# Optimization experiments

Hardware: AMD Instinct MI355X
Metric: run time of the kernel (lower is better)

Reference implementation:

```python
import jax, jax.numpy as jnp
import numpy as np

N, E, B, ROWS, IN, HID, JKO, FEAT, OH, OUT = 200000, 6400000, 64, 128, 128, 6, 4, 2560, 20, 2

def _leaky(x, s):
    return jnp.where(x >= 0, x, s * x)

def _ln(x, g, b, eps=1e-5):
    mu = jnp.mean(x, -1, keepdims=True)
    v = jnp.mean((x - mu) ** 2, -1, keepdims=True)
    return (x - mu) * jax.lax.rsqrt(v + eps) * g + b

def setup_inputs():
    key = jax.random.key(0)
    ks = jax.random.split(key, 32)
    def w(k, shape, fan_in):
        return jax.random.normal(k, shape, jnp.float32) * (1.0 / np.sqrt(fan_in))
    inp = {
        'x': jax.random.normal(ks[0], (N, IN), jnp.float32),
        'edge_index': jax.random.randint(ks[1], (2, E), 0, N, jnp.int32),
        'batch': jnp.sort(jax.random.randint(ks[2], (N,), 0, B, jnp.int32)),
        'features': jax.random.normal(ks[3], (B, ROWS, FEAT), jnp.float32),
        'one_hot': jax.random.uniform(ks[4], (B, OH), jnp.float32),
        # GATv2Conv params (heads=1)
        'W_l': w(ks[5], (IN, HID), IN), 'b_l': jnp.zeros((HID,)),
        'W_r': w(ks[6], (IN, HID), IN), 'b_r': jnp.zeros((HID,)),
        'att': w(ks[7], (HID,), HID), 'conv_b': jnp.zeros((HID,)),
        # BasicGNN final lin after JK (6 -> 4)
        'jk_W': w(ks[8], (HID, JKO), HID), 'jk_b': jnp.zeros((JKO,)),
        # MLP chain on features
        'l1_W': w(ks[9], (FEAT, 256), FEAT), 'l1_b': jnp.zeros((256,)),
        'ln1_g': jnp.ones((256,)), 'ln1_b': jnp.zeros((256,)),
        'l2_W': w(ks[10], (256, 64), 256), 'l2_b': jnp.zeros((64,)),
        'ln2_g': jnp.ones((64,)), 'ln2_b': jnp.zeros((64,)),
        'l3_W': w(ks[11], (64, 8), 64), 'l3_b': jnp.zeros((8,)),
        'ln3_g': jnp.ones((8,)), 'ln3_b': jnp.zeros((8,)),
        # flattening: rows*8 -> 32
        'fl_W': w(ks[12], (ROWS * 8, 32), ROWS * 8), 'fl_b': jnp.zeros((32,)),
        'ln4_g': jnp.ones((32,)), 'ln4_b': jnp.zeros((32,)),
        # output: 4 + 32 + 20 = 56 -> OUT
        'out_W': w(ks[13], (56, OUT), 56), 'out_b': jnp.zeros((OUT,)),
    }
    return inp

def _forward(x, features, one_hot, W_l, b_l, W_r, b_r, att, conv_b, jk_W, jk_b,
             l1_W, l1_b, ln1_g, ln1_b, l2_W, l2_b, ln2_g, ln2_b, l3_W, l3_b, ln3_g, ln3_b,
             fl_W, fl_b, ln4_g, ln4_b, out_W, out_b, edge_index, batch):
    n = x.shape[0]
    # GATv2Conv, heads=1: separate source/target transforms
    xl = x @ W_l + b_l  # [N,6] source/message features
    xr = x @ W_r + b_r  # [N,6] target features
    loops = jnp.arange(n, dtype=edge_index.dtype)
    src = jnp.concatenate([edge_index[0], loops])  # add self loops
    dst = jnp.concatenate([edge_index[1], loops])
    e = _leaky(xl[src] + xr[dst], 0.2)             # [E+N,6]
    score = e @ att                                 # [E+N]
    m = jax.lax.stop_gradient(jax.ops.segment_max(score, dst, num_segments=n))
    p = jnp.exp(score - m[dst])
    z = jax.ops.segment_sum(p, dst, num_segments=n)
    alpha = p / z[dst]                              # segment softmax over incoming edges
    agg = jax.ops.segment_sum(alpha[:, None] * xl[src], dst, num_segments=n) + conv_b
    x1 = _leaky(agg, 0.01)                          # BasicGNN act ('leakyrelu')
    # JK-LSTM with a single layer collapses to identity (softmax over 1 element)
    h = x1 @ jk_W + jk_b                            # [N,4]
    # global mean pool per graph
    nb = features.shape[0]
    sums = jax.ops.segment_sum(h, batch, num_segments=nb)
    cnt = jax.ops.segment_sum(jnp.ones((n,), h.dtype), batch, num_segments=nb)
    xgcn = sums / jnp.maximum(cnt, 1.0)[:, None]    # [B,4]
    # MLP on features (dropout = identity in eval)
    f = _leaky(_ln(features @ l1_W + l1_b, ln1_g, ln1_b), 0.01)
    f = _leaky(_ln(f @ l2_W + l2_b, ln2_g, ln2_b), 0.01)
    f = _leaky(_ln(f @ l3_W + l3_b, ln3_g, ln3_b), 0.01)  # [B,ROWS,8]
    flat = f.reshape(nb, -1)
    xf = _leaky(_ln(flat @ fl_W + fl_b, ln4_g, ln4_b), 0.01)  # [B,32]
    cat = jnp.concatenate([xgcn, xf, one_hot], axis=1)        # [B,56]
    return cat @ out_W + out_b

def reference(x, features, one_hot, W_l, b_l, W_r, b_r, att, conv_b, jk_W, jk_b,
              l1_W, l1_b, ln1_g, ln1_b, l2_W, l2_b, ln2_g, ln2_b, l3_W, l3_b, ln3_g, ln3_b,
              fl_W, fl_b, ln4_g, ln4_b, out_W, out_b, edge_index, batch):
    return _forward(x, features, one_hot, W_l, b_l, W_r, b_r, att, conv_b, jk_W, jk_b,
                    l1_W, l1_b, ln1_g, ln1_b, l2_W, l2_b, ln2_g, ln2_b, l3_W, l3_b, ln3_g, ln3_b,
                    fl_W, fl_b, ln4_g, ln4_b, out_W, out_b, edge_index, batch)
```

## Files before the change

### kernel.cpp

```cpp
#include <hip/hip_runtime.h>
#include <cstdint>
#include <cstddef>

#define N_NODES 200000
#define N_EDGES 6400000
#define NB      64
#define MROWS   8192
#define FEAT    2560

#define BSZ   256
#define NBK   782
#define EBLK  512
#define ETILE 12500
#define BCAP  8960

typedef __attribute__((ext_vector_type(8))) short bf16x8;
typedef __attribute__((ext_vector_type(4))) float f32x4;

__device__ __forceinline__ unsigned short bf16rne(float f) {
    unsigned u = __builtin_bit_cast(unsigned, f);
    u += 0x7fffu + ((u >> 16) & 1u);
    return (unsigned short)(u >> 16);
}

__device__ __forceinline__ void async_cp16(const void* g, void* l) {
    __builtin_amdgcn_global_load_lds(
        (const __attribute__((address_space(1))) unsigned int*)g,
        (__attribute__((address_space(3))) unsigned int*)l, 16, 0, 0);
}

__device__ __forceinline__ void edge_acc(
    uint4 g, const float* xrd, const float* attv, float& z, float* agg)
{
    float xls[6];
    xls[0] = __builtin_bit_cast(float, g.x << 16);
    xls[1] = __builtin_bit_cast(float, g.x & 0xffff0000u);
    xls[2] = __builtin_bit_cast(float, g.y << 16);
    xls[3] = __builtin_bit_cast(float, g.y & 0xffff0000u);
    xls[4] = __builtin_bit_cast(float, g.z << 16);
    xls[5] = __builtin_bit_cast(float, g.z & 0xffff0000u);
    float sc = 0.f;
#pragma unroll
    for (int j = 0; j < 6; j++) {
        float e = xls[j] + xrd[j];
        e = (e >= 0.f) ? e : 0.2f * e;
        sc += attv[j] * e;
    }
    const float p = __expf(sc);
    z += p;
#pragma unroll
    for (int j = 0; j < 6; j++) agg[j] += p * xls[j];
}


__global__ __launch_bounds__(256) void node_xform(
    const float* __restrict__ x,
    const float* __restrict__ Wl, const float* __restrict__ bl,
    const float* __restrict__ Wr, const float* __restrict__ br,
    unsigned short* __restrict__ xlb, float* __restrict__ xr)
{
    const int t = threadIdx.x;
    const int l = t & 15;
    const int node = blockIdx.x * 16 + (t >> 4);

    float wl[48], wr[48];
#pragma unroll
    for (int q = 0; q < 12; q++) {
        *(float4*)&wl[q * 4] = *(const float4*)(Wl + 48 * l + 4 * q);
        *(float4*)&wr[q * 4] = *(const float4*)(Wr + 48 * l + 4 * q);
    }
    float xv[8];
    *(float4*)&xv[0] = *(const float4*)(x + (size_t)node * 128 + l * 8);
    *(float4*)&xv[4] = *(const float4*)(x + (size_t)node * 128 + l * 8 + 4);

    float al[6] = {}, ar[6] = {};
#pragma unroll
    for (int i = 0; i < 8; i++) {
#pragma unroll
        for (int j = 0; j < 6; j++) {
            al[j] += xv[i] * wl[i * 6 + j];
            ar[j] += xv[i] * wr[i * 6 + j];
        }
    }
#pragma unroll
    for (int off = 8; off >= 1; off >>= 1) {
#pragma unroll
        for (int j = 0; j < 6; j++) {
            al[j] += __shfl_xor(al[j], off);
            ar[j] += __shfl_xor(ar[j], off);
        }
    }
    if (l == 0) {
        union { unsigned short h[8]; uint4 v; } u;
#pragma unroll
        for (int j = 0; j < 6; j++) u.h[j] = bf16rne(al[j] + bl[j]);
        u.h[6] = 0; u.h[7] = 0;
        *(uint4*)(xlb + (size_t)node * 8) = u.v;
        float4 r0; float2 r1;
        r0.x = ar[0] + br[0]; r0.y = ar[1] + br[1];
        r0.z = ar[2] + br[2]; r0.w = ar[3] + br[3];
        r1.x = ar[4] + br[4]; r1.y = ar[5] + br[5];
        *(float4*)(xr + (size_t)node * 8) = r0;
        *(float2*)(xr + (size_t)node * 8 + 4) = r1;
    }
}

__global__ __launch_bounds__(256) void edge_bucket(
    const int* __restrict__ ei, int* __restrict__ cursor, int* __restrict__ pairs)
{
    __shared__ int dcache[ETILE];
    __shared__ int h[NBK];
    const int t = threadIdx.x;
    const int base = blockIdx.x * ETILE;
    for (int i = t; i < NBK; i += 256) h[i] = 0;
    __syncthreads();
    for (int i = t; i < ETILE; i += 256) {
        const int d = ei[N_EDGES + base + i];
        dcache[i] = d;
        atomicAdd(&h[d >> 8], 1);
    }
    __syncthreads();
    for (int b = t; b < NBK; b += 256) {
        const int c = h[b];
        int gb = 0;
        if (c > 0) gb = atomicAdd(&cursor[b], c);
        h[b] = b * BCAP + gb;
    }
    __syncthreads();
    for (int i = t; i < ETILE; i += 256) {
        const int d = dcache[i];
        const int s = ei[base + i];
        const int pos = atomicAdd(&h[d >> 8], 1);
        pairs[pos] = (s << 8) | (d & 255);
    }
}

__global__ __launch_bounds__(256) void bucket_reduce(
    const int* __restrict__ pairs, const int* __restrict__ cursor,
    const unsigned short* __restrict__ xlb, const float* __restrict__ xr,
    const float* __restrict__ att, const float* __restrict__ conv_b,
    const float* __restrict__ jkW, const float* __restrict__ jkb,
    const int* __restrict__ batch,
    float* __restrict__ gsum, float* __restrict__ gcnt)
{
    __shared__ int sorted[BCAP];
    __shared__ int hist[256];
    __shared__ int wtot[4];
    const int t = threadIdx.x;
    const int lane = t & 63, wid = t >> 6;
    const int d0 = blockIdx.x * BSZ + t;

    float xrd[6];
    if (d0 < N_NODES) {
        float4 a = *(const float4*)(xr + (size_t)d0 * 8);
        float2 b = *(const float2*)(xr + (size_t)d0 * 8 + 4);
        xrd[0] = a.x; xrd[1] = a.y; xrd[2] = a.z;
        xrd[3] = a.w; xrd[4] = b.x; xrd[5] = b.y;
    } else {
#pragma unroll
        for (int j = 0; j < 6; j++) xrd[j] = 0.f;
    }
    float attv[6];
#pragma unroll
    for (int j = 0; j < 6; j++) attv[j] = att[j];

    float z = 0.f, agg[6] = {};
    const uint4* xl4 = (const uint4*)xlb;
    const int e0 = blockIdx.x * BCAP;
    const int e1 = e0 + cursor[blockIdx.x];

    for (int c0 = e0; c0 < e1; c0 += BCAP) {
        const int rem = e1 - c0;
        const int cnt_chunk = (rem < BCAP) ? rem : BCAP;
        hist[t] = 0;
        __syncthreads();
        for (int i = t; i < cnt_chunk; i += 256)
            atomicAdd(&hist[pairs[c0 + i] & 255], 1);
        __syncthreads();
        const int h = hist[t];
        int v = h;
#pragma unroll
        for (int d = 1; d < 64; d <<= 1) {
            int o = __shfl_up(v, d);
            if (lane >= d) v += o;
        }
        if (lane == 63) wtot[wid] = v;
        __syncthreads();
        int off = 0;
#pragma unroll
        for (int wv = 0; wv < 3; wv++) if (wv < wid) off += wtot[wv];
        const int my_start = v - h + off;
        const int my_cnt = h;
        __syncthreads();
        hist[t] = my_start;
        __syncthreads();
        for (int i = t; i < cnt_chunk; i += 256) {
            const int pv = pairs[c0 + i];
            const int pos = atomicAdd(&hist[pv & 255], 1);
            sorted[pos] = ((unsigned)pv) >> 8;
        }
        __syncthreads();
        int i = 0;
        for (; i + 4 <= my_cnt; i += 4) {
            const int s0 = sorted[my_start + i];
            const int s1 = sorted[my_start + i + 1];
            const int s2 = sorted[my_start + i + 2];
            const int s3 = sorted[my_start + i + 3];
            const uint4 g0 = xl4[s0], g1 = xl4[s1], g2 = xl4[s2], g3 = xl4[s3];
            edge_acc(g0, xrd, attv, z, agg);
            edge_acc(g1, xrd, attv, z, agg);
            edge_acc(g2, xrd, attv, z, agg);
            edge_acc(g3, xrd, attv, z, agg);
        }
        for (; i < my_cnt; i++) {
            const uint4 g = xl4[sorted[my_start + i]];
            edge_acc(g, xrd, attv, z, agg);
        }
        __syncthreads();
    }

    float hh[4] = {0.f, 0.f, 0.f, 0.f};
    float cw = 0.f;
    int b = 0;
    if (d0 < N_NODES) {
        const uint4 g = xl4[d0];
        float xld[6];
        xld[0] = __builtin_bit_cast(float, g.x << 16);
        xld[1] = __builtin_bit_cast(float, g.x & 0xffff0000u);
        xld[2] = __builtin_bit_cast(float, g.y << 16);
        xld[3] = __builtin_bit_cast(float, g.y & 0xffff0000u);
        xld[4] = __builtin_bit_cast(float, g.z << 16);
        xld[5] = __builtin_bit_cast(float, g.z & 0xffff0000u);
        float sc = 0.f;
#pragma unroll
        for (int j = 0; j < 6; j++) {
            float e = xld[j] + xrd[j];
            e = (e >= 0.f) ? e : 0.2f * e;
            sc += attv[j] * e;
        }
        const float p = __expf(sc);
        const float zz = z + p;
#pragma unroll
        for (int c = 0; c < 4; c++) hh[c] = jkb[c];
#pragma unroll
        for (int j = 0; j < 6; j++) {
            float aj = (agg[j] + p * xld[j]) / zz + conv_b[j];
            aj = (aj >= 0.f) ? aj : 0.01f * aj;
#pragma unroll
            for (int c = 0; c < 4; c++) hh[c] += aj * jkW[j * 4 + c];
        }
        b = batch[d0];
        cw = 1.f;
    }
    const int b0 = __shfl(b, 0);
    if (__all(b == b0)) {
#pragma unroll
        for (int off2 = 32; off2 >= 1; off2 >>= 1) {
#pragma unroll
            for (int c = 0; c < 4; c++) hh[c] += __shfl_xor(hh[c], off2);
            cw += __shfl_xor(cw, off2);
        }
        if (lane == 0 && cw > 0.f) {
#pragma unroll
            for (int c = 0; c < 4; c++) atomicAdd(gsum + b0 * 4 + c, hh[c]);
            atomicAdd(gcnt + b0, cw);
        }
    } else if (cw > 0.f) {
#pragma unroll
        for (int c = 0; c < 4; c++) atomicAdd(gsum + b * 4 + c, hh[c]);
        atomicAdd(gcnt + b, cw);
    }
}

__global__ __launch_bounds__(256) void castT(
    const float* __restrict__ W, unsigned short* __restrict__ Wt, int K, int N)
{
    const int k = blockIdx.x * 256 + threadIdx.x;
    const int n = blockIdx.y;
    if (k < K) Wt[(size_t)n * K + k] = bf16rne(W[(size_t)k * N + n]);
}

__global__ __launch_bounds__(256) void mfma_gemm_l1(
    const float* __restrict__ A, const unsigned short* __restrict__ Bt,
    const float* __restrict__ bias, float* __restrict__ C,
    int M, int N, int K)
{
    __shared__ unsigned short As[2][64 * 64];
    __shared__ unsigned short Bs[2][128 * 64];
    const int t = threadIdx.x;
    const int w = t >> 6, l = t & 63;
    const int l15 = l & 15, quad = l >> 4;
    const int wm = (w & 1) * 32, wn = (w >> 1) * 64;
    const int gm0 = blockIdx.x * 64;
    const int gn0 = blockIdx.y * 128;
    const int r8 = l >> 3;
    const int c8 = (l & 7) ^ r8;
    const int ar = t >> 2;
    const int ac0 = (t & 3) * 2;

    f32x4 acc[2][4];
#pragma unroll
    for (int mt = 0; mt < 2; mt++)
#pragma unroll
        for (int nt = 0; nt < 4; nt++) acc[mt][nt] = (f32x4){0.f, 0.f, 0.f, 0.f};

    const int niter = K / 64;

#pragma unroll
    for (int c = 0; c < 4; c++) {
        const int j = w * 4 + c;
        async_cp16(Bt + (size_t)(gn0 + j * 8 + r8) * K + c8 * 8, &Bs[0][j * 512]);
    }
    {
        const float* src = A + (size_t)(gm0 + ar) * K + ac0 * 8;
        float4 v0 = *(const float4*)src;
        float4 v1 = *(const float4*)(src + 4);
        float4 v2 = *(const float4*)(src + 8);
        float4 v3 = *(const float4*)(src + 12);
        union { unsigned short h[8]; uint4 u; } p0, p1;
        p0.h[0] = bf16rne(v0.x); p0.h[1] = bf16rne(v0.y);
        p0.h[2] = bf16rne(v0.z); p0.h[3] = bf16rne(v0.w);
        p0.h[4] = bf16rne(v1.x); p0.h[5] = bf16rne(v1.y);
        p0.h[6] = bf16rne(v1.z); p0.h[7] = bf16rne(v1.w);
        p1.h[0] = bf16rne(v2.x); p1.h[1] = bf16rne(v2.y);
        p1.h[2] = bf16rne(v2.z); p1.h[3] = bf16rne(v2.w);
        p1.h[4] = bf16rne(v3.x); p1.h[5] = bf16rne(v3.y);
        p1.h[6] = bf16rne(v3.z); p1.h[7] = bf16rne(v3.w);
        *(uint4*)&As[0][ar * 64 + ((ac0 + 0) ^ (ar & 7)) * 8] = p0.u;
        *(uint4*)&As[0][ar * 64 + ((ac0 + 1) ^ (ar & 7)) * 8] = p1.u;
    }

    int p = 0;
    for (int i = 0; i < niter; i++) {
        __syncthreads();
        const bool nxt = (i + 1 < niter);
        float4 v0, v1, v2, v3;
        if (nxt) {
            const int k1 = (i + 1) * 64;
#pragma unroll
            for (int c = 0; c < 4; c++) {
                const int j = w * 4 + c;
                async_cp16(Bt + (size_t)(gn0 + j * 8 + r8) * K + k1 + c8 * 8,
                           &Bs[p ^ 1][j * 512]);
            }
            const float* src = A + (size_t)(gm0 + ar) * K + k1 + ac0 * 8;
            v0 = *(const float4*)src;
            v1 = *(const float4*)(src + 4);
            v2 = *(const float4*)(src + 8);
            v3 = *(const float4*)(src + 12);
        }
#pragma unroll
        for (int kki = 0; kki < 2; kki++) {
            bf16x8 af[2], bfr[4];
#pragma unroll
            for (int mt = 0; mt < 2; mt++) {
                const int m = wm + mt * 16 + l15;
                af[mt] = *(const bf16x8*)&As[p][m * 64 + (((quad + 4 * kki) ^ (m & 7)) * 8)];
            }
#pragma unroll
            for (int nt = 0; nt < 4; nt++) {
                const int n = wn + nt * 16 + l15;
                bfr[nt] = *(const bf16x8*)&Bs[p][n * 64 + (((quad + 4 * kki) ^ (n & 7)) * 8)];
            }
#pragma unroll
            for (int mt = 0; mt < 2; mt++)
#pragma unroll
                for (int nt = 0; nt < 4; nt++)
                    acc[mt][nt] = __builtin_amdgcn_mfma_f32_16x16x32_bf16(
                        af[mt], bfr[nt], acc[mt][nt], 0, 0, 0);
        }
        if (nxt) {
            union { unsigned short h[8]; uint4 u; } p0, p1;
            p0.h[0] = bf16rne(v0.x); p0.h[1] = bf16rne(v0.y);
            p0.h[2] = bf16rne(v0.z); p0.h[3] = bf16rne(v0.w);
            p0.h[4] = bf16rne(v1.x); p0.h[5] = bf16rne(v1.y);
            p0.h[6] = bf16rne(v1.z); p0.h[7] = bf16rne(v1.w);
            p1.h[0] = bf16rne(v2.x); p1.h[1] = bf16rne(v2.y);
            p1.h[2] = bf16rne(v2.z); p1.h[3] = bf16rne(v2.w);
            p1.h[4] = bf16rne(v3.x); p1.h[5] = bf16rne(v3.y);
            p1.h[6] = bf16rne(v3.z); p1.h[7] = bf16rne(v3.w);
            *(uint4*)&As[p ^ 1][ar * 64 + ((ac0 + 0) ^ (ar & 7)) * 8] = p0.u;
            *(uint4*)&As[p ^ 1][ar * 64 + ((ac0 + 1) ^ (ar & 7)) * 8] = p1.u;
        }
        p ^= 1;
    }
#pragma unroll
    for (int nt = 0; nt < 4; nt++) {
        const int col = gn0 + wn + nt * 16 + l15;
        const float bv = bias[col];
#pragma unroll
        for (int mt = 0; mt < 2; mt++)
#pragma unroll
            for (int rr = 0; rr < 4; rr++) {
                const int row = gm0 + wm + mt * 16 + quad * 4 + rr;
                C[(size_t)row * N + col] = acc[mt][nt][rr] + bv;
            }
    }
}

__global__ __launch_bounds__(256) void mfma_gemm_l2(
    const unsigned short* __restrict__ Ab, const unsigned short* __restrict__ Bt,
    const float* __restrict__ bias, float* __restrict__ C,
    int M, int N, int K)
{
    __shared__ unsigned short As[32 * 64];
    __shared__ unsigned short Bs[64 * 64];
    const int t = threadIdx.x;
    const int w = t >> 6, l = t & 63;
    const int l15 = l & 15, quad = l >> 4;
    const int gm0 = blockIdx.x * 32;
    const int gn0 = blockIdx.y * 64;
    const int r8 = l >> 3;
    const int c8 = (l & 7) ^ r8;

    f32x4 acc[2];
    acc[0] = (f32x4){0.f, 0.f, 0.f, 0.f};
    acc[1] = (f32x4){0.f, 0.f, 0.f, 0.f};

    for (int k0 = 0; k0 < K; k0 += 64) {
#pragma unroll
        for (int c = 0; c < 2; c++) {
            const int j = w * 2 + c;
            async_cp16(Bt + (size_t)(gn0 + j * 8 + r8) * K + k0 + c8 * 8,
                       &Bs[j * 512]);
        }
        async_cp16(Ab + (size_t)(gm0 + w * 8 + r8) * K + k0 + c8 * 8, &As[w * 512]);
        __syncthreads();
#pragma unroll
        for (int kki = 0; kki < 2; kki++) {
            bf16x8 af[2], bfr;
#pragma unroll
            for (int mt = 0; mt < 2; mt++) {
                const int m = mt * 16 + l15;
                af[mt] = *(const bf16x8*)&As[m * 64 + (((quad + 4 * kki) ^ (m & 7)) * 8)];
            }
            const int n = w * 16 + l15;
            bfr = *(const bf16x8*)&Bs[n * 64 + (((quad + 4 * kki) ^ (n & 7)) * 8)];
#pragma unroll
            for (int mt = 0; mt < 2; mt++)
                acc[mt] = __builtin_amdgcn_mfma_f32_16x16x32_bf16(
                    af[mt], bfr, acc[mt], 0, 0, 0);
        }
        __syncthreads();
    }
    const int col = gn0 + w * 16 + l15;
    const float bv = bias[col];
#pragma unroll
    for (int mt = 0; mt < 2; mt++)
#pragma unroll
        for (int rr = 0; rr < 4; rr++) {
            const int row = gm0 + mt * 16 + quad * 4 + rr;
            C[(size_t)row * N + col] = acc[mt][rr] + bv;
        }
}

__global__ __launch_bounds__(256) void ln_leaky_c256(
    const float* __restrict__ f, unsigned short* __restrict__ out,
    const float* __restrict__ g, const float* __restrict__ b)
{
    const int row = blockIdx.x;
    const int t = threadIdx.x;
    float v = f[(size_t)row * 256 + t];
    float s = v, s2 = v * v;
#pragma unroll
    for (int off = 32; off >= 1; off >>= 1) {
        s += __shfl_xor(s, off);
        s2 += __shfl_xor(s2, off);
    }
    __shared__ float ws[4], ws2[4];
    const int wid = t >> 6, lane = t & 63;
    if (lane == 0) { ws[wid] = s; ws2[wid] = s2; }
    __syncthreads();
    const float S = ws[0] + ws[1] + ws[2] + ws[3];
    const float S2 = ws2[0] + ws2[1] + ws2[2] + ws2[3];
    const float mu = S * (1.0f / 256.0f);
    const float var = S2 * (1.0f / 256.0f) - mu * mu;
    float y = (v - mu) * rsqrtf(var + 1e-5f) * g[t] + b[t];
    y = (y >= 0.f) ? y : 0.01f * y;
    out[(size_t)row * 256 + t] = bf16rne(y);
}

__global__ __launch_bounds__(256) void ln_leaky_c64(
    float* __restrict__ f, const float* __restrict__ g, const float* __restrict__ b)
{
    const int wid = threadIdx.x >> 6, lane = threadIdx.x & 63;
    const int row = blockIdx.x * 4 + wid;
    float v = f[(size_t)row * 64 + lane];
    float s = v, s2 = v * v;
#pragma unroll
    for (int off = 32; off >= 1; off >>= 1) {
        s += __shfl_xor(s, off);
        s2 += __shfl_xor(s2, off);
    }
    const float mu = s * (1.0f / 64.0f);
    const float var = s2 * (1.0f / 64.0f) - mu * mu;
    float y = (v - mu) * rsqrtf(var + 1e-5f) * g[lane] + b[lane];
    f[(size_t)row * 64 + lane] = (y >= 0.f) ? y : 0.01f * y;
}

__global__ __launch_bounds__(256) void l3_ln_leaky(
    const float* __restrict__ f2, const float* __restrict__ W3,
    const float* __restrict__ b3,
    const float* __restrict__ g, const float* __restrict__ b,
    float* __restrict__ f3)
{
    __shared__ float sW[64 * 8];
    const int t = threadIdx.x;
    sW[t] = W3[t]; sW[t + 256] = W3[t + 256];
    __syncthreads();
    const int row = blockIdx.x * 32 + (t >> 3);
    const int c = t & 7;
    float acc = b3[c];
    const float* fr = f2 + (size_t)row * 64;
#pragma unroll 8
    for (int k = 0; k < 64; k++) acc += fr[k] * sW[k * 8 + c];
    float s = acc, s2 = acc * acc;
#pragma unroll
    for (int off = 4; off >= 1; off >>= 1) {
        s += __shfl_xor(s, off);
        s2 += __shfl_xor(s2, off);
    }
    const float mu = s * (1.0f / 8.0f);
    const float var = s2 * (1.0f / 8.0f) - mu * mu;
    float y = (acc - mu) * rsqrtf(var + 1e-5f) * g[c] + b[c];
    f3[(size_t)row * 8 + c] = (y >= 0.f) ? y : 0.01f * y;
}

__global__ __launch_bounds__(256) void flat_ln_leaky(
    const float* __restrict__ f3, const float* __restrict__ W,
    const float* __restrict__ bb,
    const float* __restrict__ g, const float* __restrict__ b,
    float* __restrict__ xf)
{
    __shared__ float sf[1024];
    __shared__ float sp[8][32];
    const int t = threadIdx.x;
    const int gb = blockIdx.x;
    *(float4*)&sf[t * 4] = *(const float4*)(f3 + (size_t)gb * 1024 + t * 4);
    __syncthreads();
    const int c = t & 31, part = t >> 5;
    float acc = 0.f;
    for (int k = part * 128; k < part * 128 + 128; k++) acc += sf[k] * W[k * 32 + c];
    sp[part][c] = acc;
    __syncthreads();
    if (t < 32) {
        float v = bb[t];
#pragma unroll
        for (int p = 0; p < 8; p++) v += sp[p][t];
        float s = v, s2 = v * v;
#pragma unroll
        for (int off = 16; off >= 1; off >>= 1) {
            s += __shfl_xor(s, off);
            s2 += __shfl_xor(s2, off);
        }
        const float mu = s * (1.0f / 32.0f);
        const float var = s2 * (1.0f / 32.0f) - mu * mu;
        float y = (v - mu) * rsqrtf(var + 1e-5f) * g[t] + b[t];
        xf[gb * 32 + t] = (y >= 0.f) ? y : 0.01f * y;
    }
}

__global__ __launch_bounds__(128) void final_out(
    const float* __restrict__ gsum, const float* __restrict__ gcnt,
    const float* __restrict__ xf, const float* __restrict__ onehot,
    const float* __restrict__ Wo, const float* __restrict__ bo,
    float* __restrict__ out)
{
    const int t = threadIdx.x;
    const int gb = t >> 1, o = t & 1;
    float cnt = gcnt[gb];
    cnt = (cnt > 1.f) ? cnt : 1.f;
    float acc = bo[o];
#pragma unroll
    for (int j = 0; j < 4; j++)  acc += (gsum[gb * 4 + j] / cnt) * Wo[j * 2 + o];
#pragma unroll
    for (int j = 0; j < 32; j++) acc += xf[gb * 32 + j] * Wo[(4 + j) * 2 + o];
#pragma unroll
    for (int j = 0; j < 20; j++) acc += onehot[gb * 20 + j] * Wo[(36 + j) * 2 + o];
    out[t] = acc;
}

extern "C" void kernel_launch(void* const* d_in, const int* in_sizes, int n_in,
                              void* d_out, int out_size, void* d_ws, size_t ws_size,
                              hipStream_t stream)
{
    const float* x        = (const float*)d_in[0];
    const int*   ei       = (const int*)d_in[1];
    const int*   batch    = (const int*)d_in[2];
    const float* features = (const float*)d_in[3];
    const float* one_hot  = (const float*)d_in[4];
    const float* W_l   = (const float*)d_in[5];
    const float* b_l   = (const float*)d_in[6];
    const float* W_r   = (const float*)d_in[7];
    const float* b_r   = (const float*)d_in[8];
    const float* att   = (const float*)d_in[9];
    const float* conv_b = (const float*)d_in[10];
    const float* jk_W  = (const float*)d_in[11];
    const float* jk_b  = (const float*)d_in[12];
    const float* l1_W  = (const float*)d_in[13];
    const float* l1_b  = (const float*)d_in[14];
    const float* ln1_g = (const float*)d_in[15];
    const float* ln1_b = (const float*)d_in[16];
    const float* l2_W  = (const float*)d_in[17];
    const float* l2_b  = (const float*)d_in[18];
    const float* ln2_g = (const float*)d_in[19];
    const float* ln2_b = (const float*)d_in[20];
    const float* l3_W  = (const float*)d_in[21];
    const float* l3_b  = (const float*)d_in[22];
    const float* ln3_g = (const float*)d_in[23];
    const float* ln3_b = (const float*)d_in[24];
    const float* fl_W  = (const float*)d_in[25];
    const float* fl_b  = (const float*)d_in[26];
    const float* ln4_g = (const float*)d_in[27];
    const float* ln4_b = (const float*)d_in[28];
    const float* out_W = (const float*)d_in[29];
    const float* out_b = (const float*)d_in[30];
    (void)in_sizes; (void)n_in; (void)out_size; (void)ws_size;

    float* ws = (float*)d_ws;
    unsigned short* xlb = (unsigned short*)(ws + 0);
    float* xr   = ws + 800000;
    unsigned short* w1t = (unsigned short*)(ws + 2400000);
    unsigned short* w2t = (unsigned short*)(ws + 2727680);
    float* gsum   = ws + 2735872;
    float* gcnt   = ws + 2736128;
    int*   cursor = (int*)(ws + 2736192);
    int* pairs = (int*)(ws + 2737024);
    float* f1           = ws + 2737024;
    unsigned short* f1b = (unsigned short*)(ws + 4834176);
    float* f2           = ws + 5358464;
    float* f3           = ws + 5882752;
    float* xf           = ws + 5948288;

    hipMemsetAsync(gsum, 0, 1102 * sizeof(float), stream);

    node_xform<<<N_NODES / 16, 256, 0, stream>>>(x, W_l, b_l, W_r, b_r, xlb, xr);
    edge_bucket<<<EBLK, 256, 0, stream>>>(ei, cursor, pairs);
    castT<<<dim3(10, 256), 256, 0, stream>>>(l1_W, w1t, FEAT, 256);
    castT<<<dim3(1, 64), 256, 0, stream>>>(l2_W, w2t, 256, 64);
    bucket_reduce<<<NBK, 256, 0, stream>>>(pairs, cursor, xlb, xr, att, conv_b,
                                           jk_W, jk_b, batch, gsum, gcnt);
    mfma_gemm_l1<<<dim3(MROWS / 64, 2), 256, 0, stream>>>(
        features, w1t, l1_b, f1, MROWS, 256, FEAT);
    ln_leaky_c256<<<MROWS, 256, 0, stream>>>(f1, f1b, ln1_g, ln1_b);
    mfma_gemm_l2<<<dim3(MROWS / 32, 1), 256, 0, stream>>>(
        f1b, w2t, l2_b, f2, MROWS, 64, 256);
    ln_leaky_c64<<<MROWS / 4, 256, 0, stream>>>(f2, ln2_g, ln2_b);
    l3_ln_leaky<<<MROWS / 32, 256, 0, stream>>>(f2, l3_W, l3_b, ln3_g, ln3_b, f3);
    flat_ln_leaky<<<NB, 256, 0, stream>>>(f3, fl_W, fl_b, ln4_g, ln4_b, xf);
    final_out<<<1, 128, 0, stream>>>(gsum, gcnt, xf, one_hot, out_W, out_b, (float*)d_out);
}
```

Before: 630.8 us.

## Locally sort edges in LDS before writing contiguous bucket runs to global

edge_bucket now computes a block-local prefix sum of bucket counts and scatters the edge pairs into a shared-memory sorted array. Each bucket's run is then copied to its global slot by a 16-thread group with consecutive addresses. Before, every edge was written to a random global location. The aim is to coalesce global writes to the pairs buffer, at the cost of reading the edge-index global array twice, extra LDS traffic and more barriers.

```diff
diff --git a/kernel.cpp b/kernel.cpp
--- a/kernel.cpp
+++ b/kernel.cpp
@@ -108,30 +108,78 @@
 __global__ __launch_bounds__(256) void edge_bucket(
     const int* __restrict__ ei, int* __restrict__ cursor, int* __restrict__ pairs)
 {
-    __shared__ int dcache[ETILE];
-    __shared__ int h[NBK];
-    const int t = threadIdx.x;
+    __shared__ int sorted[ETILE];
+    __shared__ int hb[NBK + 1];
+    __shared__ int cur[NBK];
+    __shared__ int gbl[NBK];
+    __shared__ int wsum[4];
+    const int t = threadIdx.x;
+    const int lane = t & 63, wid = t >> 6;
     const int base = blockIdx.x * ETILE;
-    for (int i = t; i < NBK; i += 256) h[i] = 0;
-    __syncthreads();
+
+    for (int b = t; b < NBK; b += 256) cur[b] = 0;
+    __syncthreads();
+
+    for (int i = t; i < ETILE; i += 256)
+        atomicAdd(&cur[ei[N_EDGES + base + i] >> 8], 1);
+    __syncthreads();
+
+    int c[4]; int lsum = 0;
+#pragma unroll
+    for (int q = 0; q < 4; q++) {
+        const int b = 4 * t + q;
+        c[q] = (b < NBK) ? cur[b] : 0;
+        lsum += c[q];
+    }
+    int v = lsum;
+#pragma unroll
+    for (int d = 1; d < 64; d <<= 1) {
+        const int o = __shfl_up(v, d);
+        if (lane >= d) v += o;
+    }
+    if (lane == 63) wsum[wid] = v;
+    __syncthreads();
+    int off = 0;
+#pragma unroll
+    for (int w = 0; w < 3; w++) if (w < wid) off += wsum[w];
+    int run = off + v - lsum;
+
+    int mygb[4];
+#pragma unroll
+    for (int q = 0; q < 4; q++) {
+        const int b = 4 * t + q;
+        mygb[q] = (b < NBK && c[q] > 0) ? atomicAdd(&cursor[b], c[q]) : 0;
+    }
+
+#pragma unroll
+    for (int q = 0; q < 4; q++) {
+        const int b = 4 * t + q;
+        if (b <= NBK) hb[b] = run;
+        if (b < NBK) cur[b] = run;
+        run += c[q];
+    }
+    __syncthreads();
+
     for (int i = t; i < ETILE; i += 256) {
         const int d = ei[N_EDGES + base + i];
-        dcache[i] = d;
-        atomicAdd(&h[d >> 8], 1);
-    }
-    __syncthreads();
-    for (int b = t; b < NBK; b += 256) {
-        const int c = h[b];
-        int gb = 0;
-        if (c > 0) gb = atomicAdd(&cursor[b], c);
-        h[b] = b * BCAP + gb;
-    }
-    __syncthreads();
-    for (int i = t; i < ETILE; i += 256) {
-        const int d = dcache[i];
         const int s = ei[base + i];
-        const int pos = atomicAdd(&h[d >> 8], 1);
-        pairs[pos] = (s << 8) | (d & 255);
+        const int pos = atomicAdd(&cur[d >> 8], 1);
+        sorted[pos] = (s << 8) | (d & 255);
+    }
+#pragma unroll
+    for (int q = 0; q < 4; q++) {
+        const int b = 4 * t + q;
+        if (b < NBK) gbl[b] = mygb[q];
+    }
+    __syncthreads();
+
+    const int grp = t >> 4, gl = t & 15;
+    for (int b = grp; b < NBK; b += 16) {
+        const int st = hb[b];
+        const int cnt = hb[b + 1] - st;
+        int* dst = pairs + b * BCAP + gbl[b];
+        for (int i = gl; i < cnt; i += 16)
+            dst[i] = sorted[st + i];
     }
 }
 
```

New measurement: 598.3 us. 5.2% less time.
